# Kernel optimization log

Hardware: AMD Instinct MI355X
Metric: run time of the kernel (lower is better)

## Reference

```python
import jax, jax.numpy as jnp
import numpy as np
import math

SCALE = 16.0
IGNORE_THRES = 0.5
BAD_CONF_WEIGHT = 1.25
NB, NT, NA, NH, NW, NC = 16, 50, 5, 128, 128, 20


def _inv_tanh(y):
    ys = jnp.clip(y, -1.0 + 1e-6, 1.0 - 1e-6)
    at = 0.5 * jnp.log((1.0 + ys) / (1.0 - ys))
    return jnp.where(y <= -1.0, -2.0, jnp.where(y >= 1.0, 2.0, at))


def _forward(prediction, target, target_sizes, anchors):
    nB, nA, nH, nW, _ = prediction.shape
    nC = prediction.shape[-1] - 6
    s = SCALE
    # scaled anchors and anchor corner points (matches __init__ precompute)
    aw = anchors[:, 0] / s
    ah = anchors[:, 1] / s
    ar = anchors[:, 2]
    cr, sr = jnp.cos(ar), jnp.sin(ar)
    anchor_points = jnp.stack([-cr * aw, sr * aw, cr * aw, -sr * aw,
                               -sr * ah, -cr * ah, sr * ah, cr * ah], axis=1)  # [nA,8]
    anchor_hws = (ah + aw) / 2.0

    pred_conf = prediction[..., 0]
    x = prediction[..., 1]; y = prediction[..., 2]; r = prediction[..., 3]
    h = prediction[..., 4]; w = prediction[..., 5]
    pred_cls = prediction[..., 6:]

    # ---- build_targets_dist, vectorized (original uses detached .cpu().data) ----
    tgt = jax.lax.stop_gradient(target)
    T = tgt.shape[1]
    valid = jnp.arange(T)[None, :] < target_sizes[:, None]
    gx = tgt[..., 0] / s; gy = tgt[..., 1] / s
    gw = tgt[..., 4] / s; gh = tgt[..., 3] / s
    gr = tgt[..., 2]
    valid = valid & (gw != 0) & (gh != 0)
    gi = jnp.clip(gx.astype(jnp.int32), 0, nW - 1)
    gj = jnp.clip(gy.astype(jnp.int32), 0, nH - 1)
    pts = tgt[..., 5:13] / s
    cpts = pts - jnp.tile(jnp.stack([gx, gy], axis=-1), (1, 1, 4))  # centered corners [nB,T,8]
    deltas = cpts[:, :, None, :] - anchor_points[None, None, :, :]  # [nB,T,nA,8]
    dn = sum(jnp.linalg.norm(deltas[..., i:i + 2], axis=-1) for i in (0, 2, 4, 6))
    norm = (((gh + gw) / 2.0)[:, :, None] + anchor_hws[None, None, :]) / 2.0
    anch_dists = (dn / norm) ** 2  # [nB,T,nA]

    # conf_mask: zero anchors closer than ignore_thres at (gj,gi)
    conf_mask = jnp.ones((nB, nA, nH, nW), jnp.float32)
    b3 = jnp.broadcast_to(jnp.arange(nB)[:, None, None], (nB, T, nA)).reshape(-1)
    a3 = jnp.broadcast_to(jnp.arange(nA)[None, None, :], (nB, T, nA)).reshape(-1)
    gj3 = jnp.broadcast_to(gj[:, :, None], (nB, T, nA)).reshape(-1)
    gi3 = jnp.broadcast_to(gi[:, :, None], (nB, T, nA)).reshape(-1)
    ign = ((anch_dists < IGNORE_THRES) & valid[:, :, None]).reshape(-1)
    conf_mask = conf_mask.at[b3, a3, gj3, gi3].min(jnp.where(ign, 0.0, 1.0))

    best_n = jnp.argmin(anch_dists, axis=-1)  # [nB,T]
    txv = _inv_tanh(gx - (gi.astype(jnp.float32) + 0.5))
    tyv = _inv_tanh(gy - (gj.astype(jnp.float32) + 0.5))
    rd = gr - ar[best_n]
    rd = jnp.where(rd > math.pi, rd - 2 * math.pi,
                   jnp.where(rd < -math.pi, rd + 2 * math.pi, rd))
    trv = _inv_tanh(rd / (math.pi / 2))
    twv = jnp.log(gw / aw[best_n] + 1e-16)
    thv = jnp.log(gh / ah[best_n] + 1e-16)
    tlabv = jnp.argmax(tgt[..., 13:], axis=-1)

    bS = jnp.where(valid, jnp.arange(nB)[:, None], -1).reshape(-1)  # -1 -> dropped
    idx = (bS, best_n.reshape(-1), gj.reshape(-1), gi.reshape(-1))
    z = jnp.zeros((nB, nA, nH, nW), jnp.float32)
    mask = z.at[idx].set(1.0, mode='drop')
    conf_mask = conf_mask.at[idx].set(1.0, mode='drop')
    tx = z.at[idx].set(txv.reshape(-1), mode='drop')
    ty = z.at[idx].set(tyv.reshape(-1), mode='drop')
    tw = z.at[idx].set(twv.reshape(-1), mode='drop')
    th = z.at[idx].set(thv.reshape(-1), mode='drop')
    tr = z.at[idx].set(trv.reshape(-1), mode='drop')
    tconf = mask  # tconf set to 1 exactly where mask is 1
    tlab = jnp.zeros((nB, nA, nH, nW), jnp.int32).at[idx].set(
        tlabv.reshape(-1).astype(jnp.int32), mode='drop')

    conf_mask_false = conf_mask * (1.0 - mask)

    def masked_bce(z_, t_, m_):
        l = jnp.maximum(z_, 0.0) - z_ * t_ + jnp.log1p(jnp.exp(-jnp.abs(z_)))
        return jnp.sum(l * m_) / jnp.maximum(jnp.sum(m_), 1.0)

    def masked_mse(p_, t_):
        return jnp.sum(((p_ - t_) ** 2) * mask) / jnp.maximum(jnp.sum(mask), 1.0)

    loss_conf = BAD_CONF_WEIGHT * masked_bce(pred_conf, tconf, conf_mask_false) \
        + masked_bce(pred_conf, tconf, mask)
    loss_x = masked_mse(x, tx); loss_y = masked_mse(y, ty)
    loss_w = masked_mse(w, tw); loss_h = masked_mse(h, th)
    loss_r = masked_mse(r, tr)
    logp = jax.nn.log_softmax(pred_cls, axis=-1)
    nll = -jnp.take_along_axis(logp, tlab[..., None], axis=-1)[..., 0]
    loss_cls = jnp.sum(nll * mask) / jnp.maximum(jnp.sum(mask), 1.0)
    return loss_x + loss_y + loss_w + loss_h + loss_r + loss_conf + loss_cls


def setup_inputs():
    key = jax.random.key(0)
    ks = jax.random.split(key, 8)
    s = SCALE
    prediction = jax.random.normal(ks[0], (NB, NA, NH, NW, 6 + NC), jnp.float32) * 0.5
    # targets in image pixel space (grid is NHxNW at stride SCALE)
    cx = jax.random.uniform(ks[1], (NB, NT), minval=1.0, maxval=NW - 1.0) * s
    cy = jax.random.uniform(ks[2], (NB, NT), minval=1.0, maxval=NH - 1.0) * s
    bw = jax.random.uniform(ks[3], (NB, NT), minval=8.0, maxval=96.0)
    bh = jax.random.uniform(ks[4], (NB, NT), minval=8.0, maxval=48.0)
    br = jax.random.uniform(ks[5], (NB, NT), minval=-0.3, maxval=0.3)
    c, si = jnp.cos(br), jnp.sin(br)
    pts = jnp.stack([cx - c * bw, cy + si * bw, cx + c * bw, cy - si * bw,
                     cx - si * bh, cy - c * bh, cx + si * bh, cy + c * bh], axis=-1)
    cls = jax.nn.one_hot(jax.random.randint(ks[6], (NB, NT), 0, NC), NC, dtype=jnp.float32)
    target = jnp.concatenate([jnp.stack([cx, cy, br, bh, bw], axis=-1), pts, cls], axis=-1)
    target_sizes = jax.random.randint(ks[7], (NB,), 20, NT + 1).astype(jnp.int32)
    anchors = jnp.array([[48., 16., 0.], [96., 24., 0.], [192., 32., 0.],
                         [64., 64., 0.], [32., 96., 1.5708]], jnp.float32)
    return {"prediction": prediction, "target": target,
            "target_sizes": target_sizes, "anchors": anchors}


def reference(prediction, target, target_sizes, anchors):
    return _forward(prediction, target, target_sizes, anchors)
```

## Files before the change

kernel.cpp:

```cpp
#include <hip/hip_runtime.h>
#include <math.h>

#define NBb 16
#define NTt 50
#define NAa 5
#define NHh 128
#define NWw 128
#define NCc 20
#define NCH 26
#define NCELL (NBb*NAa*NHh*NWw)
#define NFLAT (NCELL*NCH)
#define NQ4   (NFLAT/4)
#define NREC  (NBb*NTt)
#define NLIST (NREC*7)
#define SCALE_F 16.0f
#define IGNORE_THRES_F 0.5f
#define BAD_CONF_WEIGHT_F 1.25f
#define PI_F 3.14159265358979323846f

#define STATUS_OFF 16
#define REC_OFF  (STATUS_OFF + NCELL)
#define LIST_OFF (REC_OFF + 6*NREC)

__device__ __forceinline__ float inv_tanh_f(float y) {
  if (y <= -1.0f) return -2.0f;
  if (y >= 1.0f)  return  2.0f;
  float ys = fminf(fmaxf(y, -1.0f + 1e-6f), 1.0f - 1e-6f);
  return 0.5f * logf((1.0f + ys) / (1.0f - ys));
}

__device__ __forceinline__ float softplus_f(float z) {
  return fmaxf(z, 0.0f) + log1pf(expf(-fabsf(z)));
}

__global__ void k_zero(unsigned* __restrict__ wsu) {
  int stride = gridDim.x * blockDim.x;
  for (int i = blockIdx.x * blockDim.x + threadIdx.x;
       i < STATUS_OFF + NCELL; i += stride)
    wsu[i] = 0u;
}

__global__ void k_prep(const float* __restrict__ tgt,
                       const int* __restrict__ tsz,
                       const float* __restrict__ anch,
                       float* __restrict__ ws) {
  int tid = blockIdx.x * blockDim.x + threadIdx.x;
  if (tid >= NREC) return;
  int b = tid / NTt, t = tid % NTt;

  float aw[NAa], ah[NAa], ar[NAa], ahw[NAa], ap[NAa][8];
  for (int a = 0; a < NAa; ++a) {
    aw[a] = anch[a*3+0] / SCALE_F;
    ah[a] = anch[a*3+1] / SCALE_F;
    ar[a] = anch[a*3+2];
    float cr = cosf(ar[a]), sr = sinf(ar[a]);
    ap[a][0] = -cr*aw[a]; ap[a][1] =  sr*aw[a];
    ap[a][2] =  cr*aw[a]; ap[a][3] = -sr*aw[a];
    ap[a][4] = -sr*ah[a]; ap[a][5] = -cr*ah[a];
    ap[a][6] =  sr*ah[a]; ap[a][7] =  cr*ah[a];
    ahw[a] = (ah[a] + aw[a]) * 0.5f;
  }

  const float* row = tgt + (size_t)tid * (13 + NCc);
  float gx = row[0] / SCALE_F;
  float gy = row[1] / SCALE_F;
  float gr = row[2];
  float gh = row[3] / SCALE_F;
  float gw = row[4] / SCALE_F;
  bool valid = (t < tsz[b]) && (gw != 0.0f) && (gh != 0.0f);
  if (!valid) return;

  int gi = (int)gx; gi = min(max(gi, 0), NWw - 1);
  int gj = (int)gy; gj = min(max(gj, 0), NHh - 1);

  float cp[8];
  for (int k = 0; k < 8; ++k)
    cp[k] = row[5 + k] / SCALE_F - ((k & 1) ? gy : gx);

  float bestd = 1e30f; int best = 0; unsigned ignm = 0;
  for (int a = 0; a < NAa; ++a) {
    float dn = 0.0f;
    for (int p = 0; p < 8; p += 2) {
      float dx = cp[p]   - ap[a][p];
      float dy = cp[p+1] - ap[a][p+1];
      dn += sqrtf(dx*dx + dy*dy);
    }
    float nm = ((gh + gw) * 0.5f + ahw[a]) * 0.5f;
    float d = dn / nm; d = d * d;
    if (d < IGNORE_THRES_F) ignm |= (1u << a);
    if (d < bestd) { bestd = d; best = a; }
  }

  unsigned* wsu = (unsigned*)ws;
  unsigned* status = wsu + STATUS_OFF;
  unsigned* list = wsu + LIST_OFF;
  int cellbase = ((b * NAa) * NHh + gj) * NWw + gi;
  for (int a = 0; a < NAa; ++a)
    if ((ignm >> a) & 1u) {
      int cell = cellbase + a * NHh * NWw;
      atomicMax(&status[cell], 1u);
      unsigned slot = atomicAdd(&wsu[15], 1u);
      list[slot] = (unsigned)cell;
    }
  {
    int cell = cellbase + best * NHh * NWw;
    atomicMax(&status[cell], 2u + (unsigned)tid);
    if (!((ignm >> best) & 1u)) {
      unsigned slot = atomicAdd(&wsu[15], 1u);
      list[slot] = (unsigned)cell;
    }
  }

  float txv = inv_tanh_f(gx - ((float)gi + 0.5f));
  float tyv = inv_tanh_f(gy - ((float)gj + 0.5f));
  float rd = gr - ar[best];
  if (rd > PI_F) rd -= 2.0f * PI_F;
  else if (rd < -PI_F) rd += 2.0f * PI_F;
  float trv = inv_tanh_f(rd / (PI_F * 0.5f));
  float twv = logf(gw / aw[best] + 1e-16f);
  float thv = logf(gh / ah[best] + 1e-16f);
  int tlab = 0; float bm = row[13];
  for (int c = 1; c < NCc; ++c)
    if (row[13 + c] > bm) { bm = row[13 + c]; tlab = c; }

  float* rec = ws + REC_OFF;
  rec[0*NREC + tid] = txv;
  rec[1*NREC + tid] = tyv;
  rec[2*NREC + tid] = twv;
  rec[3*NREC + tid] = thv;
  rec[4*NREC + tid] = trv;
  ((int*)rec)[5*NREC + tid] = tlab;
}

__global__ void k_sum(const float4* __restrict__ pred4, float* __restrict__ ws) {
  float acc = 0.0f;
  int stride = gridDim.x * blockDim.x;
  for (int q = blockIdx.x * blockDim.x + threadIdx.x; q < NQ4; q += stride) {
    float4 v = pred4[q];
    int m13 = q % 13;
    if (m13 == 0)      acc += softplus_f(v.x);
    else if (m13 == 6) acc += softplus_f(v.z);
  }
  for (int off = 32; off; off >>= 1) acc += __shfl_down(acc, off, 64);
  __shared__ float s0[8];
  int wid = threadIdx.x >> 6, lane = threadIdx.x & 63;
  if (lane == 0) s0[wid] = acc;
  __syncthreads();
  if (threadIdx.x == 0) {
    float a = 0.0f;
    int nw = blockDim.x >> 6;
    for (int w = 0; w < nw; ++w) a += s0[w];
    atomicAdd(ws + 0, a);
  }
}

__global__ void __launch_bounds__(1024) k_fixfin(const float* __restrict__ pred,
                                                 float* __restrict__ ws,
                                                 float* __restrict__ out) {
  unsigned* wsu = (unsigned*)ws;
  unsigned* status = wsu + STATUS_OFF;
  const unsigned* list = wsu + LIST_OFF;
  const float* rec = ws + REC_OFF;
  int nlist = (int)wsu[15];

  float sub = 0.0f, cnb = 0.0f, obj = 0.0f;
  float sx = 0.0f, sy = 0.0f, sw = 0.0f, sh = 0.0f, sr = 0.0f;
  float scls = 0.0f, cm = 0.0f;

  for (int i = threadIdx.x; i < nlist; i += 1024) {
    unsigned cell = list[i];
    unsigned st = atomicExch(&status[cell], 0u);
    if (st == 0u) continue;
    const float* cp = pred + (size_t)cell * NCH;
    float z = cp[0];
    sub += softplus_f(z);
    cnb += 1.0f;
    if (st >= 2u) {
      int r = (int)(st - 2u);
      obj += softplus_f(z) - z;
      float dx = cp[1] - rec[0*NREC + r];
      float dy = cp[2] - rec[1*NREC + r];
      float dr = cp[3] - rec[4*NREC + r];
      float dh = cp[4] - rec[3*NREC + r];
      float dw = cp[5] - rec[2*NREC + r];
      sx += dx*dx; sy += dy*dy; sw += dw*dw; sh += dh*dh; sr += dr*dr;
      int tlab = ((const int*)rec)[5*NREC + r];
      float m = cp[6];
      for (int c = 1; c < NCc; ++c) m = fmaxf(m, cp[6 + c]);
      float s = 0.0f;
      for (int c = 0; c < NCc; ++c) s += expf(cp[6 + c] - m);
      scls += (m + logf(s)) - cp[6 + tlab];
      cm += 1.0f;
    }
  }

  float vals[10] = {sub, cnb, obj, sx, sy, sw, sh, sr, scls, cm};
  __shared__ float red[16][10];
  int wid = threadIdx.x >> 6, lane = threadIdx.x & 63;
  for (int k = 0; k < 10; ++k) {
    float v = vals[k];
    for (int off = 32; off; off >>= 1) v += __shfl_down(v, off, 64);
    if (lane == 0) red[wid][k] = v;
    vals[k] = v;
  }
  __syncthreads();
  if (threadIdx.x == 0) {
    float tot[10];
    for (int k = 0; k < 10; ++k) {
      float v = 0.0f;
      for (int w = 0; w < 16; ++w) v += red[w][k];
      tot[k] = v;
    }
    float acc_bg = ws[0] - tot[0];
    float cnt_bg = (float)NCELL - tot[1];
    float db = fmaxf(cnt_bg, 1.0f);
    float dm = fmaxf(tot[9], 1.0f);
    float loss_conf = BAD_CONF_WEIGHT_F * (acc_bg / db) + tot[2] / dm;
    out[0] = (tot[3] + tot[4] + tot[5] + tot[6] + tot[7] + tot[8]) / dm + loss_conf;
  }
}

extern "C" void kernel_launch(void* const* d_in, const int* in_sizes, int n_in,
                              void* d_out, int out_size, void* d_ws, size_t ws_size,
                              hipStream_t stream) {
  const float* pred = (const float*)d_in[0];
  const float* tgt  = (const float*)d_in[1];
  const int*   tsz  = (const int*)d_in[2];
  const float* anch = (const float*)d_in[3];
  float* ws = (float*)d_ws;

  k_zero<<<1280, 256, 0, stream>>>((unsigned*)ws);
  k_prep<<<4, 256, 0, stream>>>(tgt, tsz, anch, ws);
  k_sum<<<4096, 256, 0, stream>>>((const float4*)pred, ws);
  k_fixfin<<<1, 1024, 0, stream>>>(pred, ws, (float*)d_out);
}
```

Measured before the change: 242.8 us.

## Fuse conf-softplus sum with fixup pass, reading only conf channel

Replaces the full-tensor float4 scan with a kernel where each thread reads just the conf element of five cells, and merges the fix-up list processing into the same grid-wide kernel. Per-block partials are accumulated with atomics and finalised in a small separate kernel. This aims to cut the bytes read from the prediction tensor and remove the single-block serial fix-up. The strided scalar reads still fetch whole cache lines, so some bandwidth is wasted.

```diff
diff --git a/kernel.cpp b/kernel.cpp
--- a/kernel.cpp
+++ b/kernel.cpp
@@ -9,8 +9,6 @@
 #define NCc 20
 #define NCH 26
 #define NCELL (NBb*NAa*NHh*NWw)
-#define NFLAT (NCELL*NCH)
-#define NQ4   (NFLAT/4)
 #define NREC  (NBb*NTt)
 #define NLIST (NREC*7)
 #define SCALE_F 16.0f
@@ -22,6 +20,12 @@
 #define REC_OFF  (STATUS_OFF + NCELL)
 #define LIST_OFF (REC_OFF + 6*NREC)
 
+#define MAIN_GRID 1024
+#define MAIN_BLK  256
+#define MAIN_STRIDE (MAIN_GRID*MAIN_BLK)
+static_assert(NCELL == 5 * MAIN_STRIDE, "conf loop unroll assumes 5 cells/thread");
+static_assert(((STATUS_OFF + NCELL) & 3) == 0, "k_zero uint4 alignment");
+
 __device__ __forceinline__ float inv_tanh_f(float y) {
   if (y <= -1.0f) return -2.0f;
   if (y >= 1.0f)  return  2.0f;
@@ -33,11 +37,11 @@
   return fmaxf(z, 0.0f) + log1pf(expf(-fabsf(z)));
 }
 
-__global__ void k_zero(unsigned* __restrict__ wsu) {
+__global__ void k_zero(uint4* __restrict__ ws4) {
+  const int n4 = (STATUS_OFF + NCELL) / 4;
   int stride = gridDim.x * blockDim.x;
-  for (int i = blockIdx.x * blockDim.x + threadIdx.x;
-       i < STATUS_OFF + NCELL; i += stride)
-    wsu[i] = 0u;
+  for (int i = blockIdx.x * blockDim.x + threadIdx.x; i < n4; i += stride)
+    ws4[i] = make_uint4(0u, 0u, 0u, 0u);
 }
 
 __global__ void k_prep(const float* __restrict__ tgt,
@@ -132,42 +136,27 @@
   ((int*)rec)[5*NREC + tid] = tlab;
 }
 
-__global__ void k_sum(const float4* __restrict__ pred4, float* __restrict__ ws) {
-  float acc = 0.0f;
-  int stride = gridDim.x * blockDim.x;
-  for (int q = blockIdx.x * blockDim.x + threadIdx.x; q < NQ4; q += stride) {
-    float4 v = pred4[q];
-    int m13 = q % 13;
-    if (m13 == 0)      acc += softplus_f(v.x);
-    else if (m13 == 6) acc += softplus_f(v.z);
-  }
-  for (int off = 32; off; off >>= 1) acc += __shfl_down(acc, off, 64);
-  __shared__ float s0[8];
-  int wid = threadIdx.x >> 6, lane = threadIdx.x & 63;
-  if (lane == 0) s0[wid] = acc;
-  __syncthreads();
-  if (threadIdx.x == 0) {
-    float a = 0.0f;
-    int nw = blockDim.x >> 6;
-    for (int w = 0; w < nw; ++w) a += s0[w];
-    atomicAdd(ws + 0, a);
-  }
-}
-
-__global__ void __launch_bounds__(1024) k_fixfin(const float* __restrict__ pred,
-                                                 float* __restrict__ ws,
-                                                 float* __restrict__ out) {
+__global__ void __launch_bounds__(MAIN_BLK) k_main(const float* __restrict__ pred,
+                                                   float* __restrict__ ws) {
   unsigned* wsu = (unsigned*)ws;
   unsigned* status = wsu + STATUS_OFF;
   const unsigned* list = wsu + LIST_OFF;
   const float* rec = ws + REC_OFF;
   int nlist = (int)wsu[15];
+  int t = blockIdx.x * MAIN_BLK + threadIdx.x;
+
+  float acc = 0.0f;
+  #pragma unroll
+  for (int k = 0; k < 5; ++k) {
+    float z = pred[(size_t)(t + k * MAIN_STRIDE) * NCH];
+    acc += softplus_f(z);
+  }
 
   float sub = 0.0f, cnb = 0.0f, obj = 0.0f;
   float sx = 0.0f, sy = 0.0f, sw = 0.0f, sh = 0.0f, sr = 0.0f;
   float scls = 0.0f, cm = 0.0f;
 
-  for (int i = threadIdx.x; i < nlist; i += 1024) {
+  for (int i = t; i < nlist; i += MAIN_STRIDE) {
     unsigned cell = list[i];
     unsigned st = atomicExch(&status[cell], 0u);
     if (st == 0u) continue;
@@ -194,29 +183,34 @@
     }
   }
 
-  float vals[10] = {sub, cnb, obj, sx, sy, sw, sh, sr, scls, cm};
-  __shared__ float red[16][10];
+  float vals[11] = {acc, sub, cnb, obj, sx, sy, sw, sh, sr, scls, cm};
+  __shared__ float red[4][11];
   int wid = threadIdx.x >> 6, lane = threadIdx.x & 63;
-  for (int k = 0; k < 10; ++k) {
+  #pragma unroll
+  for (int k = 0; k < 11; ++k) {
     float v = vals[k];
     for (int off = 32; off; off >>= 1) v += __shfl_down(v, off, 64);
     if (lane == 0) red[wid][k] = v;
-    vals[k] = v;
   }
   __syncthreads();
+  if (threadIdx.x < 11) {
+    float v = red[0][threadIdx.x] + red[1][threadIdx.x]
+            + red[2][threadIdx.x] + red[3][threadIdx.x];
+    if (v != 0.0f) atomicAdd(ws + threadIdx.x, v);
+  }
+}
+
+__global__ void k_fin(const float* __restrict__ ws, float* __restrict__ out) {
   if (threadIdx.x == 0) {
-    float tot[10];
-    for (int k = 0; k < 10; ++k) {
-      float v = 0.0f;
-      for (int w = 0; w < 16; ++w) v += red[w][k];
-      tot[k] = v;
-    }
-    float acc_bg = ws[0] - tot[0];
-    float cnt_bg = (float)NCELL - tot[1];
+    float acc = ws[0], sub = ws[1], cnb = ws[2], obj = ws[3];
+    float sx = ws[4], sy = ws[5], sw = ws[6], sh = ws[7], sr = ws[8];
+    float scls = ws[9], cm = ws[10];
+    float acc_bg = acc - sub;
+    float cnt_bg = (float)NCELL - cnb;
     float db = fmaxf(cnt_bg, 1.0f);
-    float dm = fmaxf(tot[9], 1.0f);
-    float loss_conf = BAD_CONF_WEIGHT_F * (acc_bg / db) + tot[2] / dm;
-    out[0] = (tot[3] + tot[4] + tot[5] + tot[6] + tot[7] + tot[8]) / dm + loss_conf;
+    float dm = fmaxf(cm, 1.0f);
+    float loss_conf = BAD_CONF_WEIGHT_F * (acc_bg / db) + obj / dm;
+    out[0] = (sx + sy + sw + sh + sr + scls) / dm + loss_conf;
   }
 }
 
@@ -229,8 +223,8 @@
   const float* anch = (const float*)d_in[3];
   float* ws = (float*)d_ws;
 
-  k_zero<<<1280, 256, 0, stream>>>((unsigned*)ws);
+  k_zero<<<320, 256, 0, stream>>>((uint4*)ws);
   k_prep<<<4, 256, 0, stream>>>(tgt, tsz, anch, ws);
-  k_sum<<<4096, 256, 0, stream>>>((const float4*)pred, ws);
-  k_fixfin<<<1, 1024, 0, stream>>>(pred, ws, (float*)d_out);
-}
+  k_main<<<MAIN_GRID, MAIN_BLK, 0, stream>>>(pred, ws);
+  k_fin<<<1, 64, 0, stream>>>(ws, (float*)d_out);
+}
```

Measured after the change: 215.3 us. 1.13x faster.
